# Performance work log

Measured on AMD Instinct MI355X. Metric: run time of the kernel, lower is better.

## Reference

```python
import jax, jax.numpy as jnp
import numpy as np

N_NODES = 100000
N_EDGES = 1600000
D_FEAT = 128
HIDDEN = 16
N_CLASSES = 16


def setup_inputs() -> dict:
    key = jax.random.key(0)
    ks = jax.random.split(key, 6)
    x = jax.random.normal(ks[0], (N_NODES, D_FEAT), dtype=jnp.float32)
    edge_index = jax.random.randint(ks[1], (2, N_EDGES), 0, N_NODES, dtype=jnp.int64)
    # Glorot-ish scaled weights
    w1_rel = jax.random.normal(ks[2], (D_FEAT, HIDDEN), dtype=jnp.float32) / np.sqrt(D_FEAT)
    w1_root = jax.random.normal(ks[3], (D_FEAT, HIDDEN), dtype=jnp.float32) / np.sqrt(D_FEAT)
    b1 = jnp.zeros((HIDDEN,), dtype=jnp.float32)
    w2_rel = jax.random.normal(ks[4], (HIDDEN, N_CLASSES), dtype=jnp.float32) / np.sqrt(HIDDEN)
    w2_root = jax.random.normal(ks[5], (HIDDEN, N_CLASSES), dtype=jnp.float32) / np.sqrt(HIDDEN)
    b2 = jnp.zeros((N_CLASSES,), dtype=jnp.float32)
    return {"x": x, "edge_index": edge_index, "w1_rel": w1_rel, "w1_root": w1_root,
            "b1": b1, "w2_rel": w2_rel, "w2_root": w2_root, "b2": b2}


def _graph_conv(x, src, dst, w_rel, w_root, b):
    # PyG GraphConv(aggr='add'): out_i = lin_rel(sum_{j->i} x_j) + lin_root(x_i)
    n = x.shape[0]
    agg = jax.ops.segment_sum(x[src], dst, num_segments=n)  # [N, d_in]
    return agg @ w_rel + x @ w_root + b


def reference(x, edge_index, w1_rel, w1_root, b1, w2_rel, w2_root, b2):
    src, dst = edge_index[0], edge_index[1]
    h = jax.nn.relu(_graph_conv(x, src, dst, w1_rel, w1_root, b1))
    # F.dropout(training=False) -> identity in eval mode
    out = _graph_conv(h, src, dst, w2_rel, w2_root, b2)
    return jax.nn.log_softmax(out, axis=1)
```

## Files before the change

kernel.cpp:

```cpp
#include <hip/hip_runtime.h>

#define DFEAT 128
#define HID 16
#define BKT_NODES 128
#define BKT_SHIFT 7
#define CAP 2432
#define CAPI 10
#define CHUNK 4096
#define NOEDGE 0xFFFFFFFFu

typedef __attribute__((ext_vector_type(8))) short short8;
typedef __attribute__((ext_vector_type(4))) float floatx4;

__device__ __forceinline__ float bf2f(unsigned v) { return __uint_as_float(v << 16); }
__device__ __forceinline__ unsigned short f2bf(float f) {
    unsigned u = __float_as_uint(f);
    return (unsigned short)((u + 0x7FFFu + ((u >> 16) & 1u)) >> 16);
}
__device__ __forceinline__ unsigned pack2(float a, float b) {
    return (unsigned)f2bf(a) | ((unsigned)f2bf(b) << 16);
}

__global__ __launch_bounds__(512) void k_detect(const unsigned short* __restrict__ x,
                                                const int* __restrict__ ei,
                                                int* __restrict__ flags,
                                                int* __restrict__ gcur, int nbkt) {
    const int t = threadIdx.x;
    for (int i = t; i < nbkt; i += 512) gcur[i] = 0;
    if (t < 64) {
        unsigned short v = x[2 * t];
        int e = (v >> 7) & 0xFF;
        bool okbf = (v == 0) || (e >= 110 && e <= 130);
        unsigned long long mbf = __ballot(okbf);
        bool z = (ei[2 * t + 1] == 0);
        unsigned long long mz = __ballot(z);
        if (t == 0) {
            flags[0] = (__popcll(mbf) >= 52) ? 1 : 0;
            flags[1] = (__popcll(mz) >= 60) ? 1 : 0;
        }
    }
}

__global__ __launch_bounds__(256) void k_pl(const int* __restrict__ ei,
                                            unsigned* __restrict__ eb,
                                            int* __restrict__ gcur,
                                            const void* __restrict__ xv,
                                            const void* __restrict__ wrel,
                                            const void* __restrict__ wroot,
                                            unsigned short* __restrict__ p1b,
                                            unsigned short* __restrict__ q1b,
                                            const int* __restrict__ flags,
                                            int E, int nbkt, int N, int nPart) {
    __shared__ int hist[1024];
    const int t = threadIdx.x;

    if ((int)blockIdx.x < nPart) {
        for (int i = t; i < nbkt; i += 256) hist[i] = 0;
        __syncthreads();
        const int base = blockIdx.x * CHUNK;
        const int i64 = flags[1];
        unsigned pk[16];
        unsigned short bk[16];
        if (i64 && !(E & 1)) {
#pragma unroll
            for (int ip = 0; ip < 8; ++ip) {
                int e = base + ip * 512 + 2 * t;
                if (e < E) {
                    int4 sv = *(const int4*)(ei + 2 * (size_t)e);
                    int4 dv = *(const int4*)(ei + 2 * ((size_t)E + e));
                    int b0 = dv.x >> BKT_SHIFT;
                    pk[2 * ip] = ((unsigned)sv.x << BKT_SHIFT) | (unsigned)(dv.x & (BKT_NODES - 1));
                    bk[2 * ip] = (unsigned short)b0;
                    atomicAdd(&hist[b0], 1);
                    int b1 = dv.z >> BKT_SHIFT;
                    pk[2 * ip + 1] = ((unsigned)sv.z << BKT_SHIFT) | (unsigned)(dv.z & (BKT_NODES - 1));
                    bk[2 * ip + 1] = (unsigned short)b1;
                    atomicAdd(&hist[b1], 1);
                } else {
                    bk[2 * ip] = 0xFFFFu;
                    bk[2 * ip + 1] = 0xFFFFu;
                }
            }
        } else {
#pragma unroll
            for (int i = 0; i < 16; ++i) {
                int e = base + i * 256 + t;
                if (e < E) {
                    int src, dst;
                    if (i64) { src = ei[2 * (size_t)e]; dst = ei[2 * ((size_t)E + e)]; }
                    else     { src = ei[e];             dst = ei[(size_t)E + e]; }
                    int b = dst >> BKT_SHIFT;
                    pk[i] = ((unsigned)src << BKT_SHIFT) | (unsigned)(dst & (BKT_NODES - 1));
                    bk[i] = (unsigned short)b;
                    atomicAdd(&hist[b], 1);
                } else {
                    bk[i] = 0xFFFFu;
                }
            }
        }
        __syncthreads();
        for (int b = t; b < nbkt; b += 256) {
            int c = hist[b];
            hist[b] = c ? atomicAdd(&gcur[b], c) : 0;
        }
        __syncthreads();
#pragma unroll
        for (int i = 0; i < 16; ++i) {
            if (bk[i] != 0xFFFFu) {
                int pos = atomicAdd(&hist[bk[i]], 1);
                if (pos >= 0 && pos < CAP)
                    eb[(size_t)bk[i] * CAP + pos] = pk[i];
            }
        }
        return;
    }

    const int lane = t & 63, wave = t >> 6;
    const int bf = flags[0];
    const int m = lane & 15;
    const int quad = lane >> 4;
    const int nodebase = ((int)blockIdx.x - nPart) * 64 + wave * 16;

    short8 Brel[4], Broot[4];
    if (bf) {
        const unsigned short* a = (const unsigned short*)wrel;
        const unsigned short* c = (const unsigned short*)wroot;
#pragma unroll
        for (int kb = 0; kb < 4; ++kb) {
            short8 br, bo;
#pragma unroll
            for (int j = 0; j < 8; ++j) {
                int k = kb * 32 + quad * 8 + j;
                br[j] = (short)a[k * HID + m];
                bo[j] = (short)c[k * HID + m];
            }
            Brel[kb] = br; Broot[kb] = bo;
        }
    } else {
        const float* a = (const float*)wrel;
        const float* c = (const float*)wroot;
#pragma unroll
        for (int kb = 0; kb < 4; ++kb) {
            short8 br, bo;
#pragma unroll
            for (int j = 0; j < 8; ++j) {
                int k = kb * 32 + quad * 8 + j;
                br[j] = (short)f2bf(a[k * HID + m]);
                bo[j] = (short)f2bf(c[k * HID + m]);
            }
            Brel[kb] = br; Broot[kb] = bo;
        }
    }

    int row = nodebase + m;
    if (row >= N) row = N - 1;

    floatx4 accP = {0.f, 0.f, 0.f, 0.f}, accQ = {0.f, 0.f, 0.f, 0.f};
    if (bf) {
        const unsigned short* xp = (const unsigned short*)xv;
        const unsigned short* rp = xp + (size_t)row * DFEAT + quad * 8;
#pragma unroll
        for (int kb = 0; kb < 4; ++kb) {
            short8 A = *(const short8*)(rp + kb * 32);
            accP = __builtin_amdgcn_mfma_f32_16x16x32_bf16(A, Brel[kb], accP, 0, 0, 0);
            accQ = __builtin_amdgcn_mfma_f32_16x16x32_bf16(A, Broot[kb], accQ, 0, 0, 0);
        }
    } else {
        const float* xp = (const float*)xv;
        const float* rp = xp + (size_t)row * DFEAT + quad * 8;
#pragma unroll
        for (int kb = 0; kb < 4; ++kb) {
            float4 v0 = *(const float4*)(rp + kb * 32);
            float4 v1 = *(const float4*)(rp + kb * 32 + 4);
            short8 A;
            A[0] = (short)f2bf(v0.x); A[1] = (short)f2bf(v0.y);
            A[2] = (short)f2bf(v0.z); A[3] = (short)f2bf(v0.w);
            A[4] = (short)f2bf(v1.x); A[5] = (short)f2bf(v1.y);
            A[6] = (short)f2bf(v1.z); A[7] = (short)f2bf(v1.w);
            accP = __builtin_amdgcn_mfma_f32_16x16x32_bf16(A, Brel[kb], accP, 0, 0, 0);
            accQ = __builtin_amdgcn_mfma_f32_16x16x32_bf16(A, Broot[kb], accQ, 0, 0, 0);
        }
    }

#pragma unroll
    for (int r = 0; r < 4; ++r) {
        int node = nodebase + quad * 4 + r;
        if (node < N) {
            p1b[(size_t)node * HID + m] = f2bf(accP[r]);
            q1b[(size_t)node * HID + m] = f2bf(accQ[r]);
        }
    }
}

__global__ __launch_bounds__(256) void k_sagg1(const unsigned* __restrict__ eb,
                                               const int* __restrict__ gcur,
                                               const unsigned short* __restrict__ p1b,
                                               const unsigned short* __restrict__ q1b,
                                               const void* __restrict__ b1,
                                               const void* __restrict__ w2rel,
                                               const void* __restrict__ w2root,
                                               unsigned short* __restrict__ p2b,
                                               unsigned short* __restrict__ q2b,
                                               unsigned* __restrict__ csr,
                                               int* __restrict__ offsets,
                                               int* __restrict__ ends,
                                               const int* __restrict__ flags,
                                               int N) {
    __shared__ unsigned srt[CAP];
    __shared__ int cnts[BKT_NODES];
    __shared__ int offs[BKT_NODES];
    __shared__ float4 swp[HID][8];
    __shared__ float sb[HID];
    const int t = threadIdx.x;
    const int b = blockIdx.x;
    const int bf = flags[0];

    if (t < 128) {
        int k = t >> 3, p = t & 7;
        float4 w;
        if (bf) {
            const unsigned short* a = (const unsigned short*)w2rel;
            const unsigned short* c = (const unsigned short*)w2root;
            w = make_float4(bf2f(a[k * 16 + 2 * p]), bf2f(a[k * 16 + 2 * p + 1]),
                            bf2f(c[k * 16 + 2 * p]), bf2f(c[k * 16 + 2 * p + 1]));
        } else {
            const float* a = (const float*)w2rel;
            const float* c = (const float*)w2root;
            w = make_float4(a[k * 16 + 2 * p], a[k * 16 + 2 * p + 1],
                            c[k * 16 + 2 * p], c[k * 16 + 2 * p + 1]);
        }
        swp[k][p] = w;
    }
    if (t < HID) sb[t] = bf ? bf2f(((const unsigned short*)b1)[t]) : ((const float*)b1)[t];
    if (t < BKT_NODES) cnts[t] = 0;
    __syncthreads();

    int cnt = gcur[b];
    if (cnt < 0) cnt = 0;
    if (cnt > CAP) cnt = CAP;
    const unsigned* ep = eb + (size_t)b * CAP;

    unsigned ev[CAPI];
    int rk[CAPI];
#pragma unroll
    for (int i = 0; i < CAPI; ++i) {
        int e = i * 256 + t;
        if (e < cnt) {
            unsigned w = ep[e];
            ev[i] = w;
            rk[i] = atomicAdd(&cnts[w & (BKT_NODES - 1u)], 1);
        } else ev[i] = NOEDGE;
    }
    __syncthreads();
    if (t < BKT_NODES) offs[t] = cnts[t];
    __syncthreads();
    for (int off = 1; off < BKT_NODES; off <<= 1) {
        int v = 0;
        if (t >= off && t < BKT_NODES) v = offs[t - off];
        __syncthreads();
        if (t < BKT_NODES) offs[t] += v;
        __syncthreads();
    }
#pragma unroll
    for (int i = 0; i < CAPI; ++i) {
        if (ev[i] != NOEDGE) {
            unsigned local = ev[i] & (BKT_NODES - 1u);
            int pos = offs[local] - cnts[local] + rk[i];
            srt[pos] = ev[i] >> BKT_SHIFT;
        }
    }
    __syncthreads();

    const int base = b * CAP;
    for (int e = t; e < cnt; e += 256) csr[base + e] = srt[e];
    const int gb = b * BKT_NODES;
    if (t < BKT_NODES) {
        int gn = gb + t;
        if (gn < N) {
            offsets[gn] = base + offs[t] - cnts[t];
            ends[gn]    = base + offs[t];
        }
    }

    const int grp = t >> 3, jp = t & 7;
#pragma unroll
    for (int g = 0; g < 4; ++g) {
        int node = g * 32 + grp;
        int gn = gb + node;
        int beg = offs[node] - cnts[node];
        int end = offs[node];
        float2 acc = make_float2(0.f, 0.f);
        int e = beg;
        for (; e + 4 <= end; e += 4) {
            unsigned s0 = srt[e], s1 = srt[e + 1], s2 = srt[e + 2], s3 = srt[e + 3];
            unsigned u0 = *(const unsigned*)(p1b + (size_t)s0 * HID + 2 * jp);
            unsigned u1 = *(const unsigned*)(p1b + (size_t)s1 * HID + 2 * jp);
            unsigned u2 = *(const unsigned*)(p1b + (size_t)s2 * HID + 2 * jp);
            unsigned u3 = *(const unsigned*)(p1b + (size_t)s3 * HID + 2 * jp);
            acc.x += bf2f(u0 & 0xFFFFu) + bf2f(u1 & 0xFFFFu)
                   + bf2f(u2 & 0xFFFFu) + bf2f(u3 & 0xFFFFu);
            acc.y += bf2f(u0 >> 16) + bf2f(u1 >> 16) + bf2f(u2 >> 16) + bf2f(u3 >> 16);
        }
        for (; e < end; ++e) {
            unsigned u = *(const unsigned*)(p1b + (size_t)srt[e] * HID + 2 * jp);
            acc.x += bf2f(u & 0xFFFFu);
            acc.y += bf2f(u >> 16);
        }
        float hx = 0.f, hy = 0.f;
        if (gn < N) {
            unsigned qu = *(const unsigned*)(q1b + (size_t)gn * HID + 2 * jp);
            hx = fmaxf(acc.x + bf2f(qu & 0xFFFFu) + sb[2 * jp], 0.f);
            hy = fmaxf(acc.y + bf2f(qu >> 16) + sb[2 * jp + 1], 0.f);
        }
        float2 sp = make_float2(0.f, 0.f), sq = make_float2(0.f, 0.f);
#pragma unroll
        for (int k = 0; k < HID; ++k) {
            float hsel = (k & 1) ? hy : hx;
            float hk = __shfl(hsel, k >> 1, 8);
            float4 w = swp[k][jp];
            sp.x += hk * w.x; sp.y += hk * w.y;
            sq.x += hk * w.z; sq.y += hk * w.w;
        }
        if (gn < N) {
            ((unsigned*)p2b)[(size_t)gn * 8 + jp] = pack2(sp.x, sp.y);
            ((unsigned*)q2b)[(size_t)gn * 8 + jp] = pack2(sq.x, sq.y);
        }
    }
}

__global__ __launch_bounds__(256) void k_agg2(const int* __restrict__ offsets,
                                              const int* __restrict__ ends,
                                              const unsigned* __restrict__ csr,
                                              const unsigned short* __restrict__ p2b,
                                              const unsigned short* __restrict__ q2b,
                                              const void* __restrict__ b2,
                                              void* __restrict__ out,
                                              const int* __restrict__ flags,
                                              int N) {
    __shared__ float sb[HID];
    const int t = threadIdx.x;
    const int bf = flags[0];
    if (t < HID) sb[t] = bf ? bf2f(((const unsigned short*)b2)[t]) : ((const float*)b2)[t];
    __syncthreads();

    const int grp = t >> 3, jp = t & 7;
    const int n = blockIdx.x * 32 + grp;
    if (n >= N) return;

    const int beg = offsets[n], end = ends[n];
    float2 acc = make_float2(0.f, 0.f);
    int e = beg;
    for (; e + 8 <= end; e += 8) {
        unsigned s0 = csr[e],     s1 = csr[e + 1], s2 = csr[e + 2], s3 = csr[e + 3];
        unsigned s4 = csr[e + 4], s5 = csr[e + 5], s6 = csr[e + 6], s7 = csr[e + 7];
        unsigned u0 = *(const unsigned*)(p2b + (size_t)s0 * HID + 2 * jp);
        unsigned u1 = *(const unsigned*)(p2b + (size_t)s1 * HID + 2 * jp);
        unsigned u2 = *(const unsigned*)(p2b + (size_t)s2 * HID + 2 * jp);
        unsigned u3 = *(const unsigned*)(p2b + (size_t)s3 * HID + 2 * jp);
        unsigned u4 = *(const unsigned*)(p2b + (size_t)s4 * HID + 2 * jp);
        unsigned u5 = *(const unsigned*)(p2b + (size_t)s5 * HID + 2 * jp);
        unsigned u6 = *(const unsigned*)(p2b + (size_t)s6 * HID + 2 * jp);
        unsigned u7 = *(const unsigned*)(p2b + (size_t)s7 * HID + 2 * jp);
        acc.x += bf2f(u0 & 0xFFFFu) + bf2f(u1 & 0xFFFFu)
               + bf2f(u2 & 0xFFFFu) + bf2f(u3 & 0xFFFFu)
               + bf2f(u4 & 0xFFFFu) + bf2f(u5 & 0xFFFFu)
               + bf2f(u6 & 0xFFFFu) + bf2f(u7 & 0xFFFFu);
        acc.y += bf2f(u0 >> 16) + bf2f(u1 >> 16) + bf2f(u2 >> 16) + bf2f(u3 >> 16)
               + bf2f(u4 >> 16) + bf2f(u5 >> 16) + bf2f(u6 >> 16) + bf2f(u7 >> 16);
    }
    for (; e + 2 <= end; e += 2) {
        unsigned s0 = csr[e], s1 = csr[e + 1];
        unsigned u0 = *(const unsigned*)(p2b + (size_t)s0 * HID + 2 * jp);
        unsigned u1 = *(const unsigned*)(p2b + (size_t)s1 * HID + 2 * jp);
        acc.x += bf2f(u0 & 0xFFFFu) + bf2f(u1 & 0xFFFFu);
        acc.y += bf2f(u0 >> 16) + bf2f(u1 >> 16);
    }
    for (; e < end; ++e) {
        unsigned u = *(const unsigned*)(p2b + (size_t)csr[e] * HID + 2 * jp);
        acc.x += bf2f(u & 0xFFFFu);
        acc.y += bf2f(u >> 16);
    }
    unsigned qu = *(const unsigned*)(q2b + (size_t)n * HID + 2 * jp);
    float ox = acc.x + bf2f(qu & 0xFFFFu) + sb[2 * jp];
    float oy = acc.y + bf2f(qu >> 16) + sb[2 * jp + 1];

    float m = fmaxf(ox, oy);
#pragma unroll
    for (int mask = 1; mask < 8; mask <<= 1) m = fmaxf(m, __shfl_xor(m, mask, 8));
    float s = __expf(ox - m) + __expf(oy - m);
#pragma unroll
    for (int mask = 1; mask < 8; mask <<= 1) s += __shfl_xor(s, mask, 8);
    const float l = m + __logf(s);

    if (bf) ((unsigned*)out)[(size_t)n * 8 + jp] = pack2(ox - l, oy - l);
    else    ((float2*)out)[(size_t)n * 8 + jp] = make_float2(ox - l, oy - l);
}

extern "C" void kernel_launch(void* const* d_in, const int* in_sizes, int n_in,
                              void* d_out, int out_size, void* d_ws, size_t ws_size,
                              hipStream_t stream) {
    const void* x       = d_in[0];
    const int*  ei      = (const int*)d_in[1];
    const void* w1_rel  = d_in[2];
    const void* w1_root = d_in[3];
    const void* b1      = d_in[4];
    const void* w2_rel  = d_in[5];
    const void* w2_root = d_in[6];
    const void* b2      = d_in[7];

    const int N = in_sizes[0] / DFEAT;
    const int E = in_sizes[1] / 2;
    const int nbkt = (N + BKT_NODES - 1) / BKT_NODES;

    unsigned short* p1b = (unsigned short*)d_ws;
    unsigned short* q1b = p1b + (size_t)N * HID;
    unsigned short* p2b = q1b + (size_t)N * HID;
    unsigned short* q2b = p2b + (size_t)N * HID;
    unsigned* eb   = (unsigned*)(q2b + (size_t)N * HID);
    unsigned* csr  = eb + (size_t)nbkt * CAP;
    int* offsets   = (int*)(csr + (size_t)nbkt * CAP);
    int* ends      = offsets + N;
    int* gcur      = ends + N;
    int* flags     = gcur + nbkt;

    const int nPart = (E + CHUNK - 1) / CHUNK;
    const int nLin  = (N + 63) / 64;

    k_detect<<<1, 512, 0, stream>>>((const unsigned short*)x, ei, flags, gcur, nbkt);
    k_pl<<<nPart + nLin, 256, 0, stream>>>(ei, eb, gcur, x, w1_rel, w1_root,
                                           p1b, q1b, flags, E, nbkt, N, nPart);
    k_sagg1<<<nbkt, 256, 0, stream>>>(eb, gcur, p1b, q1b, b1, w2_rel, w2_root,
                                      p2b, q2b, csr, offsets, ends, flags, N);
    k_agg2<<<(N + 31) / 32, 256, 0, stream>>>(offsets, ends, csr, p2b, q2b, b2,
                                              d_out, flags, N);
}
```

Before: 164.5 us.

## Fuse both aggregation layers into one cooperative kernel with a grid sync

Replaces the separate layer-1 aggregation kernel and layer-2 gather kernel with one cooperative kernel. Each block keeps its locally sorted bucket edge list in shared memory and, after a grid-wide sync, reuses it for the second aggregation and the log-softmax. This drops the global CSR/offsets write and re-read and one kernel launch. In exchange it adds a grid barrier, atomic loads for cross-block visibility of p2b, and a requirement that all buckets be co-resident. The old two-kernel path remains as a fallback if the cooperative launch fails.

```diff
diff --git a/kernel.cpp b/kernel.cpp
--- a/kernel.cpp
+++ b/kernel.cpp
@@ -1,4 +1,7 @@
 #include <hip/hip_runtime.h>
+#include <hip/hip_cooperative_groups.h>
+
+namespace cg = cooperative_groups;
 
 #define DFEAT 128
 #define HID 16
@@ -19,6 +22,12 @@
 }
 __device__ __forceinline__ unsigned pack2(float a, float b) {
     return (unsigned)f2bf(a) | ((unsigned)f2bf(b) << 16);
+}
+__device__ __forceinline__ unsigned ald(const unsigned* p) {
+    return __hip_atomic_load(p, __ATOMIC_RELAXED, __HIP_MEMORY_SCOPE_AGENT);
+}
+__device__ __forceinline__ void ast(unsigned* p, unsigned v) {
+    __hip_atomic_store(p, v, __ATOMIC_RELAXED, __HIP_MEMORY_SCOPE_AGENT);
 }
 
 __global__ __launch_bounds__(512) void k_detect(const unsigned short* __restrict__ x,
@@ -188,6 +197,197 @@
         if (node < N) {
             p1b[(size_t)node * HID + m] = f2bf(accP[r]);
             q1b[(size_t)node * HID + m] = f2bf(accQ[r]);
+        }
+    }
+}
+
+__global__ __launch_bounds__(256) void k_sagg(const unsigned* __restrict__ eb,
+                                              const int* __restrict__ gcur,
+                                              const unsigned short* __restrict__ p1b,
+                                              const unsigned short* __restrict__ q1b,
+                                              const void* __restrict__ b1,
+                                              const void* __restrict__ w2rel,
+                                              const void* __restrict__ w2root,
+                                              unsigned short* __restrict__ p2b,
+                                              unsigned short* __restrict__ q2b,
+                                              const void* __restrict__ b2,
+                                              void* __restrict__ out,
+                                              const int* __restrict__ flags,
+                                              int N) {
+    __shared__ unsigned srt[CAP];
+    __shared__ int cnts[BKT_NODES];
+    __shared__ int offs[BKT_NODES];
+    __shared__ float4 swp[HID][8];
+    __shared__ float sb[HID];
+    __shared__ float sb2[HID];
+    const int t = threadIdx.x;
+    const int b = blockIdx.x;
+    const int bf = flags[0];
+
+    if (t < 128) {
+        int k = t >> 3, p = t & 7;
+        float4 w;
+        if (bf) {
+            const unsigned short* a = (const unsigned short*)w2rel;
+            const unsigned short* c = (const unsigned short*)w2root;
+            w = make_float4(bf2f(a[k * 16 + 2 * p]), bf2f(a[k * 16 + 2 * p + 1]),
+                            bf2f(c[k * 16 + 2 * p]), bf2f(c[k * 16 + 2 * p + 1]));
+        } else {
+            const float* a = (const float*)w2rel;
+            const float* c = (const float*)w2root;
+            w = make_float4(a[k * 16 + 2 * p], a[k * 16 + 2 * p + 1],
+                            c[k * 16 + 2 * p], c[k * 16 + 2 * p + 1]);
+        }
+        swp[k][p] = w;
+    }
+    if (t < HID) {
+        sb[t]  = bf ? bf2f(((const unsigned short*)b1)[t]) : ((const float*)b1)[t];
+        sb2[t] = bf ? bf2f(((const unsigned short*)b2)[t]) : ((const float*)b2)[t];
+    }
+    if (t < BKT_NODES) cnts[t] = 0;
+    __syncthreads();
+
+    int cnt = gcur[b];
+    if (cnt < 0) cnt = 0;
+    if (cnt > CAP) cnt = CAP;
+    const unsigned* ep = eb + (size_t)b * CAP;
+
+    unsigned ev[CAPI];
+    int rk[CAPI];
+#pragma unroll
+    for (int i = 0; i < CAPI; ++i) {
+        int e = i * 256 + t;
+        if (e < cnt) {
+            unsigned w = ep[e];
+            ev[i] = w;
+            rk[i] = atomicAdd(&cnts[w & (BKT_NODES - 1u)], 1);
+        } else ev[i] = NOEDGE;
+    }
+    __syncthreads();
+    if (t < BKT_NODES) offs[t] = cnts[t];
+    __syncthreads();
+    for (int off = 1; off < BKT_NODES; off <<= 1) {
+        int v = 0;
+        if (t >= off && t < BKT_NODES) v = offs[t - off];
+        __syncthreads();
+        if (t < BKT_NODES) offs[t] += v;
+        __syncthreads();
+    }
+#pragma unroll
+    for (int i = 0; i < CAPI; ++i) {
+        if (ev[i] != NOEDGE) {
+            unsigned local = ev[i] & (BKT_NODES - 1u);
+            int pos = offs[local] - cnts[local] + rk[i];
+            srt[pos] = ev[i] >> BKT_SHIFT;
+        }
+    }
+    __syncthreads();
+
+    const int gb = b * BKT_NODES;
+    const int grp = t >> 3, jp = t & 7;
+
+#pragma unroll
+    for (int g = 0; g < 4; ++g) {
+        int node = g * 32 + grp;
+        int gn = gb + node;
+        int beg = offs[node] - cnts[node];
+        int end = offs[node];
+        float2 acc = make_float2(0.f, 0.f);
+        int e = beg;
+        for (; e + 4 <= end; e += 4) {
+            unsigned s0 = srt[e], s1 = srt[e + 1], s2 = srt[e + 2], s3 = srt[e + 3];
+            unsigned u0 = *(const unsigned*)(p1b + (size_t)s0 * HID + 2 * jp);
+            unsigned u1 = *(const unsigned*)(p1b + (size_t)s1 * HID + 2 * jp);
+            unsigned u2 = *(const unsigned*)(p1b + (size_t)s2 * HID + 2 * jp);
+            unsigned u3 = *(const unsigned*)(p1b + (size_t)s3 * HID + 2 * jp);
+            acc.x += bf2f(u0 & 0xFFFFu) + bf2f(u1 & 0xFFFFu)
+                   + bf2f(u2 & 0xFFFFu) + bf2f(u3 & 0xFFFFu);
+            acc.y += bf2f(u0 >> 16) + bf2f(u1 >> 16) + bf2f(u2 >> 16) + bf2f(u3 >> 16);
+        }
+        for (; e < end; ++e) {
+            unsigned u = *(const unsigned*)(p1b + (size_t)srt[e] * HID + 2 * jp);
+            acc.x += bf2f(u & 0xFFFFu);
+            acc.y += bf2f(u >> 16);
+        }
+        float hx = 0.f, hy = 0.f;
+        if (gn < N) {
+            unsigned qu = *(const unsigned*)(q1b + (size_t)gn * HID + 2 * jp);
+            hx = fmaxf(acc.x + bf2f(qu & 0xFFFFu) + sb[2 * jp], 0.f);
+            hy = fmaxf(acc.y + bf2f(qu >> 16) + sb[2 * jp + 1], 0.f);
+        }
+        float2 sp = make_float2(0.f, 0.f), sq = make_float2(0.f, 0.f);
+#pragma unroll
+        for (int k = 0; k < HID; ++k) {
+            float hsel = (k & 1) ? hy : hx;
+            float hk = __shfl(hsel, k >> 1, 8);
+            float4 w = swp[k][jp];
+            sp.x += hk * w.x; sp.y += hk * w.y;
+            sq.x += hk * w.z; sq.y += hk * w.w;
+        }
+        if (gn < N) {
+            ast((unsigned*)p2b + (size_t)gn * 8 + jp, pack2(sp.x, sp.y));
+            ((unsigned*)q2b)[(size_t)gn * 8 + jp] = pack2(sq.x, sq.y);
+        }
+    }
+
+    __threadfence();
+    cg::this_grid().sync();
+
+#pragma unroll
+    for (int g = 0; g < 4; ++g) {
+        int node = g * 32 + grp;
+        int gn = gb + node;
+        int beg = offs[node] - cnts[node];
+        int end = offs[node];
+        float2 acc = make_float2(0.f, 0.f);
+        const unsigned* pb = (const unsigned*)p2b;
+        int e = beg;
+        for (; e + 8 <= end; e += 8) {
+            unsigned s0 = srt[e],     s1 = srt[e + 1], s2 = srt[e + 2], s3 = srt[e + 3];
+            unsigned s4 = srt[e + 4], s5 = srt[e + 5], s6 = srt[e + 6], s7 = srt[e + 7];
+            unsigned u0 = ald(pb + (size_t)s0 * 8 + jp);
+            unsigned u1 = ald(pb + (size_t)s1 * 8 + jp);
+            unsigned u2 = ald(pb + (size_t)s2 * 8 + jp);
+            unsigned u3 = ald(pb + (size_t)s3 * 8 + jp);
+            unsigned u4 = ald(pb + (size_t)s4 * 8 + jp);
+            unsigned u5 = ald(pb + (size_t)s5 * 8 + jp);
+            unsigned u6 = ald(pb + (size_t)s6 * 8 + jp);
+            unsigned u7 = ald(pb + (size_t)s7 * 8 + jp);
+            acc.x += bf2f(u0 & 0xFFFFu) + bf2f(u1 & 0xFFFFu)
+                   + bf2f(u2 & 0xFFFFu) + bf2f(u3 & 0xFFFFu)
+                   + bf2f(u4 & 0xFFFFu) + bf2f(u5 & 0xFFFFu)
+                   + bf2f(u6 & 0xFFFFu) + bf2f(u7 & 0xFFFFu);
+            acc.y += bf2f(u0 >> 16) + bf2f(u1 >> 16) + bf2f(u2 >> 16) + bf2f(u3 >> 16)
+                   + bf2f(u4 >> 16) + bf2f(u5 >> 16) + bf2f(u6 >> 16) + bf2f(u7 >> 16);
+        }
+        for (; e + 2 <= end; e += 2) {
+            unsigned s0 = srt[e], s1 = srt[e + 1];
+            unsigned u0 = ald(pb + (size_t)s0 * 8 + jp);
+            unsigned u1 = ald(pb + (size_t)s1 * 8 + jp);
+            acc.x += bf2f(u0 & 0xFFFFu) + bf2f(u1 & 0xFFFFu);
+            acc.y += bf2f(u0 >> 16) + bf2f(u1 >> 16);
+        }
+        for (; e < end; ++e) {
+            unsigned u = ald(pb + (size_t)srt[e] * 8 + jp);
+            acc.x += bf2f(u & 0xFFFFu);
+            acc.y += bf2f(u >> 16);
+        }
+        float ox = 0.f, oy = 0.f;
+        if (gn < N) {
+            unsigned qu = *(const unsigned*)(q2b + (size_t)gn * HID + 2 * jp);
+            ox = acc.x + bf2f(qu & 0xFFFFu) + sb2[2 * jp];
+            oy = acc.y + bf2f(qu >> 16) + sb2[2 * jp + 1];
+        }
+        float m = fmaxf(ox, oy);
+#pragma unroll
+        for (int mask = 1; mask < 8; mask <<= 1) m = fmaxf(m, __shfl_xor(m, mask, 8));
+        float s = __expf(ox - m) + __expf(oy - m);
+#pragma unroll
+        for (int mask = 1; mask < 8; mask <<= 1) s += __shfl_xor(s, mask, 8);
+        const float l = m + __logf(s);
+        if (gn < N) {
+            if (bf) ((unsigned*)out)[(size_t)gn * 8 + jp] = pack2(ox - l, oy - l);
+            else    ((float2*)out)[(size_t)gn * 8 + jp] = make_float2(ox - l, oy - l);
         }
     }
 }
@@ -429,8 +629,35 @@
     k_detect<<<1, 512, 0, stream>>>((const unsigned short*)x, ei, flags, gcur, nbkt);
     k_pl<<<nPart + nLin, 256, 0, stream>>>(ei, eb, gcur, x, w1_rel, w1_root,
                                            p1b, q1b, flags, E, nbkt, N, nPart);
-    k_sagg1<<<nbkt, 256, 0, stream>>>(eb, gcur, p1b, q1b, b1, w2_rel, w2_root,
-                                      p2b, q2b, csr, offsets, ends, flags, N);
-    k_agg2<<<(N + 31) / 32, 256, 0, stream>>>(offsets, ends, csr, p2b, q2b, b2,
-                                              d_out, flags, N);
-}
+
+    int dev = 0, coop = 0;
+    hipGetDevice(&dev);
+    hipDeviceGetAttribute(&coop, hipDeviceAttributeCooperativeLaunch, dev);
+
+    hipError_t err = hipErrorUnknown;
+    if (coop) {
+        const unsigned* eb_a        = eb;
+        const int* gcur_a           = gcur;
+        const unsigned short* p1b_a = p1b;
+        const unsigned short* q1b_a = q1b;
+        const void* b1_a            = b1;
+        const void* w2rel_a         = w2_rel;
+        const void* w2root_a        = w2_root;
+        unsigned short* p2b_a       = p2b;
+        unsigned short* q2b_a       = q2b;
+        const void* b2_a            = b2;
+        void* out_a                 = d_out;
+        const int* flags_a          = flags;
+        int N_a                     = N;
+        void* args[] = {&eb_a, &gcur_a, &p1b_a, &q1b_a, &b1_a, &w2rel_a, &w2root_a,
+                        &p2b_a, &q2b_a, &b2_a, &out_a, &flags_a, &N_a};
+        err = hipLaunchCooperativeKernel((void*)k_sagg, dim3(nbkt), dim3(256),
+                                         args, 0, stream);
+    }
+    if (err != hipSuccess) {
+        k_sagg1<<<nbkt, 256, 0, stream>>>(eb, gcur, p1b, q1b, b1, w2_rel, w2_root,
+                                          p2b, q2b, csr, offsets, ends, flags, N);
+        k_agg2<<<(N + 31) / 32, 256, 0, stream>>>(offsets, ends, csr, p2b, q2b, b2,
+                                                  d_out, flags, N);
+    }
+}
```

New measurement: 347.2 us. 111% more time.

## Halve bucket size and partition chunk; process two node tiles per wave in linear

Applied to the files above, without the earlier changes.

Bucket width drops from 128 to 64 nodes, with capacity and the partition chunk halved to match. This doubles the number of buckets and sort blocks and shrinks per-block shared-memory sort work. The fused linear part now has each wave compute two 16-row MFMA tiles, reusing the weight registers and issuing more loads before the MFMAs. Risks are the larger histogram (nbkt may exceed 2048 only for bigger graphs), more global atomics on gcur, and a tighter bucket capacity that could overflow on skewed degree distributions.

```diff
diff --git a/kernel.cpp b/kernel.cpp
--- a/kernel.cpp
+++ b/kernel.cpp
@@ -2,11 +2,11 @@
 
 #define DFEAT 128
 #define HID 16
-#define BKT_NODES 128
-#define BKT_SHIFT 7
-#define CAP 2432
-#define CAPI 10
-#define CHUNK 4096
+#define BKT_NODES 64
+#define BKT_SHIFT 6
+#define CAP 1280
+#define CAPI 5
+#define CHUNK 2048
 #define NOEDGE 0xFFFFFFFFu
 
 typedef __attribute__((ext_vector_type(8))) short short8;
@@ -51,7 +51,7 @@
                                             unsigned short* __restrict__ q1b,
                                             const int* __restrict__ flags,
                                             int E, int nbkt, int N, int nPart) {
-    __shared__ int hist[1024];
+    __shared__ int hist[2048];
     const int t = threadIdx.x;
 
     if ((int)blockIdx.x < nPart) {
@@ -59,11 +59,11 @@
         __syncthreads();
         const int base = blockIdx.x * CHUNK;
         const int i64 = flags[1];
-        unsigned pk[16];
-        unsigned short bk[16];
+        unsigned pk[8];
+        unsigned short bk[8];
         if (i64 && !(E & 1)) {
 #pragma unroll
-            for (int ip = 0; ip < 8; ++ip) {
+            for (int ip = 0; ip < 4; ++ip) {
                 int e = base + ip * 512 + 2 * t;
                 if (e < E) {
                     int4 sv = *(const int4*)(ei + 2 * (size_t)e);
@@ -83,7 +83,7 @@
             }
         } else {
 #pragma unroll
-            for (int i = 0; i < 16; ++i) {
+            for (int i = 0; i < 8; ++i) {
                 int e = base + i * 256 + t;
                 if (e < E) {
                     int src, dst;
@@ -105,7 +105,7 @@
         }
         __syncthreads();
 #pragma unroll
-        for (int i = 0; i < 16; ++i) {
+        for (int i = 0; i < 8; ++i) {
             if (bk[i] != 0xFFFFu) {
                 int pos = atomicAdd(&hist[bk[i]], 1);
                 if (pos >= 0 && pos < CAP)
@@ -119,7 +119,7 @@
     const int bf = flags[0];
     const int m = lane & 15;
     const int quad = lane >> 4;
-    const int nodebase = ((int)blockIdx.x - nPart) * 64 + wave * 16;
+    const int nodebase = ((int)blockIdx.x - nPart) * 128 + wave * 32;
 
     short8 Brel[4], Broot[4];
     if (bf) {
@@ -152,42 +152,64 @@
         }
     }
 
-    int row = nodebase + m;
-    if (row >= N) row = N - 1;
-
-    floatx4 accP = {0.f, 0.f, 0.f, 0.f}, accQ = {0.f, 0.f, 0.f, 0.f};
+    int row0 = nodebase + m;           if (row0 >= N) row0 = N - 1;
+    int row1 = nodebase + 16 + m;      if (row1 >= N) row1 = N - 1;
+
+    floatx4 accP0 = {0.f, 0.f, 0.f, 0.f}, accQ0 = {0.f, 0.f, 0.f, 0.f};
+    floatx4 accP1 = {0.f, 0.f, 0.f, 0.f}, accQ1 = {0.f, 0.f, 0.f, 0.f};
     if (bf) {
         const unsigned short* xp = (const unsigned short*)xv;
-        const unsigned short* rp = xp + (size_t)row * DFEAT + quad * 8;
+        const unsigned short* rp0 = xp + (size_t)row0 * DFEAT + quad * 8;
+        const unsigned short* rp1 = xp + (size_t)row1 * DFEAT + quad * 8;
+        short8 A0[4], A1[4];
+#pragma unroll
+        for (int kb = 0; kb < 4; ++kb) A0[kb] = *(const short8*)(rp0 + kb * 32);
+#pragma unroll
+        for (int kb = 0; kb < 4; ++kb) A1[kb] = *(const short8*)(rp1 + kb * 32);
 #pragma unroll
         for (int kb = 0; kb < 4; ++kb) {
-            short8 A = *(const short8*)(rp + kb * 32);
-            accP = __builtin_amdgcn_mfma_f32_16x16x32_bf16(A, Brel[kb], accP, 0, 0, 0);
-            accQ = __builtin_amdgcn_mfma_f32_16x16x32_bf16(A, Broot[kb], accQ, 0, 0, 0);
+            accP0 = __builtin_amdgcn_mfma_f32_16x16x32_bf16(A0[kb], Brel[kb], accP0, 0, 0, 0);
+            accQ0 = __builtin_amdgcn_mfma_f32_16x16x32_bf16(A0[kb], Broot[kb], accQ0, 0, 0, 0);
+            accP1 = __builtin_amdgcn_mfma_f32_16x16x32_bf16(A1[kb], Brel[kb], accP1, 0, 0, 0);
+            accQ1 = __builtin_amdgcn_mfma_f32_16x16x32_bf16(A1[kb], Broot[kb], accQ1, 0, 0, 0);
         }
     } else {
         const float* xp = (const float*)xv;
-        const float* rp = xp + (size_t)row * DFEAT + quad * 8;
+        const float* rp0 = xp + (size_t)row0 * DFEAT + quad * 8;
+        const float* rp1 = xp + (size_t)row1 * DFEAT + quad * 8;
 #pragma unroll
         for (int kb = 0; kb < 4; ++kb) {
-            float4 v0 = *(const float4*)(rp + kb * 32);
-            float4 v1 = *(const float4*)(rp + kb * 32 + 4);
-            short8 A;
-            A[0] = (short)f2bf(v0.x); A[1] = (short)f2bf(v0.y);
-            A[2] = (short)f2bf(v0.z); A[3] = (short)f2bf(v0.w);
-            A[4] = (short)f2bf(v1.x); A[5] = (short)f2bf(v1.y);
-            A[6] = (short)f2bf(v1.z); A[7] = (short)f2bf(v1.w);
-            accP = __builtin_amdgcn_mfma_f32_16x16x32_bf16(A, Brel[kb], accP, 0, 0, 0);
-            accQ = __builtin_amdgcn_mfma_f32_16x16x32_bf16(A, Broot[kb], accQ, 0, 0, 0);
+            float4 v0 = *(const float4*)(rp0 + kb * 32);
+            float4 v1 = *(const float4*)(rp0 + kb * 32 + 4);
+            float4 w0 = *(const float4*)(rp1 + kb * 32);
+            float4 w1 = *(const float4*)(rp1 + kb * 32 + 4);
+            short8 A0, A1;
+            A0[0] = (short)f2bf(v0.x); A0[1] = (short)f2bf(v0.y);
+            A0[2] = (short)f2bf(v0.z); A0[3] = (short)f2bf(v0.w);
+            A0[4] = (short)f2bf(v1.x); A0[5] = (short)f2bf(v1.y);
+            A0[6] = (short)f2bf(v1.z); A0[7] = (short)f2bf(v1.w);
+            A1[0] = (short)f2bf(w0.x); A1[1] = (short)f2bf(w0.y);
+            A1[2] = (short)f2bf(w0.z); A1[3] = (short)f2bf(w0.w);
+            A1[4] = (short)f2bf(w1.x); A1[5] = (short)f2bf(w1.y);
+            A1[6] = (short)f2bf(w1.z); A1[7] = (short)f2bf(w1.w);
+            accP0 = __builtin_amdgcn_mfma_f32_16x16x32_bf16(A0, Brel[kb], accP0, 0, 0, 0);
+            accQ0 = __builtin_amdgcn_mfma_f32_16x16x32_bf16(A0, Broot[kb], accQ0, 0, 0, 0);
+            accP1 = __builtin_amdgcn_mfma_f32_16x16x32_bf16(A1, Brel[kb], accP1, 0, 0, 0);
+            accQ1 = __builtin_amdgcn_mfma_f32_16x16x32_bf16(A1, Broot[kb], accQ1, 0, 0, 0);
         }
     }
 
 #pragma unroll
     for (int r = 0; r < 4; ++r) {
-        int node = nodebase + quad * 4 + r;
-        if (node < N) {
-            p1b[(size_t)node * HID + m] = f2bf(accP[r]);
-            q1b[(size_t)node * HID + m] = f2bf(accQ[r]);
+        int node0 = nodebase + quad * 4 + r;
+        if (node0 < N) {
+            p1b[(size_t)node0 * HID + m] = f2bf(accP0[r]);
+            q1b[(size_t)node0 * HID + m] = f2bf(accQ0[r]);
+        }
+        int node1 = nodebase + 16 + quad * 4 + r;
+        if (node1 < N) {
+            p1b[(size_t)node1 * HID + m] = f2bf(accP1[r]);
+            q1b[(size_t)node1 * HID + m] = f2bf(accQ1[r]);
         }
     }
 }
@@ -284,7 +306,7 @@
 
     const int grp = t >> 3, jp = t & 7;
 #pragma unroll
-    for (int g = 0; g < 4; ++g) {
+    for (int g = 0; g < 2; ++g) {
         int node = g * 32 + grp;
         int gn = gb + node;
         int beg = offs[node] - cnts[node];
@@ -424,7 +446,7 @@
     int* flags     = gcur + nbkt;
 
     const int nPart = (E + CHUNK - 1) / CHUNK;
-    const int nLin  = (N + 63) / 64;
+    const int nLin  = (N + 127) / 128;
 
     k_detect<<<1, 512, 0, stream>>>((const unsigned short*)x, ei, flags, gcur, nbkt);
     k_pl<<<nPart + nLin, 256, 0, stream>>>(ei, eb, gcur, x, w1_rel, w1_root,
```

Measured after the change: 183.1 us. +11.3%, slower.
